# Optimization experiments

Measured on AMD Instinct MI355X. Metric: run time of the kernel, lower is better.

## Reference

```python
import jax, jax.numpy as jnp
import numpy as np

H, DH = 8, 32          # heads, per-head dim
C = H * DH             # channels = 256
N = 20000              # nodes
E = 160000             # edges per relation
L = 4                  # layers
R = 2                  # edge types


def setup_inputs() -> dict:
    key = jax.random.key(0)
    ks = jax.random.split(key, 8)
    return {
        "x": jax.random.normal(ks[0], (N, C), jnp.float32),
        "ei0": jax.random.randint(ks[1], (2, E), 0, N, jnp.int32),
        "ei1": jax.random.randint(ks[2], (2, E), 0, N, jnp.int32),
        "kqv_w": jax.random.normal(ks[3], (L, C, 3 * C), jnp.float32) * 0.05,
        "kqv_b": jnp.zeros((L, 3 * C), jnp.float32),
        "out_w": jax.random.normal(ks[4], (L, C, C), jnp.float32) * 0.05,
        "out_b": jnp.zeros((L, C), jnp.float32),
        "skip": jnp.ones((L,), jnp.float32),
        "krel": jax.random.normal(ks[5], (L, R, H, DH, DH), jnp.float32) * 0.1,
        "vrel": jax.random.normal(ks[6], (L, R, H, DH, DH), jnp.float32) * 0.1,
        "prel": jnp.ones((L, R, H), jnp.float32),
        "ln_g": jnp.ones((L - 1, C), jnp.float32),
        "ln_b": jnp.zeros((L - 1, C), jnp.float32),
    }


def _segment_softmax(logits, seg, n):
    m = jax.ops.segment_max(logits, seg, num_segments=n)
    m = jnp.where(jnp.isfinite(m), m, 0.0)  # empty segments -> avoid -inf
    e = jnp.exp(logits - m[seg])
    s = jax.ops.segment_sum(e, seg, num_segments=n)
    return e / jnp.maximum(s[seg], 1e-16)


def _hgt_conv(x, edge_list, kqv_w, kqv_b, out_w, out_b, skip, krel, vrel, prel):
    n = x.shape[0]
    kqv = x @ kqv_w + kqv_b                       # [N, 3C]
    k, q, v = jnp.split(kqv, 3, axis=1)
    k = k.reshape(n, H, DH)
    q = q.reshape(n, H, DH)
    v = v.reshape(n, H, DH)
    logits, msgs, dsts = [], [], []
    for r, ei in enumerate(edge_list):            # loop over fixed small relation set
        src, dst = ei[0], ei[1]
        k_e = jnp.einsum('ehd,hdf->ehf', k[src], krel[r])   # relation-specific keys
        v_e = jnp.einsum('ehd,hdf->ehf', v[src], vrel[r])   # relation-specific values
        a = (q[dst] * k_e).sum(-1) * prel[r] / np.sqrt(DH)  # [E, H]
        logits.append(a)
        msgs.append(v_e)
        dsts.append(dst)
    logits = jnp.concatenate(logits, 0)
    msgs = jnp.concatenate(msgs, 0)
    dst = jnp.concatenate(dsts, 0)
    # softmax per destination node over ALL incoming edge types jointly (PyG HGTConv)
    alpha = _segment_softmax(logits, dst, n)      # [Etot, H]
    agg = jax.ops.segment_sum(msgs * alpha[:, :, None], dst, num_segments=n)
    agg = agg.reshape(n, C)
    a_out = jax.nn.gelu(agg, approximate=False) @ out_w + out_b
    s = jax.nn.sigmoid(skip)                      # skip applies: out dim == in dim
    return s * a_out + (1.0 - s) * x


def _layer_norm(h, g, b, eps=1e-5):
    mu = h.mean(-1, keepdims=True)
    var = ((h - mu) ** 2).mean(-1, keepdims=True)
    return (h - mu) * jax.lax.rsqrt(var + eps) * g + b


def reference(x, ei0, ei1, kqv_w, kqv_b, out_w, out_b, skip, krel, vrel, prel, ln_g, ln_b):
    edge_list = [ei0, ei1]
    h = x
    for i in range(L):
        h = _hgt_conv(h, edge_list, kqv_w[i], kqv_b[i], out_w[i], out_b[i],
                      skip[i], krel[i], vrel[i], prel[i])
        if i < L - 1:
            h = jax.nn.relu(h)
            h = _layer_norm(h, ln_g[i], ln_b[i])
            # dropout: identity in eval mode (p irrelevant at inference)
    return h
```

## Files before the change

kernel.cpp:

```cpp
#include <hip/hip_runtime.h>
#include <math.h>

#define NN 20000
#define NPAD 20096
#define CC 256
#define HH 8
#define EE 160000
#define TE 320000
#define KVSTRIDE 512
#define APAN ((size_t)NPAD*32)
#define BPAN 40960
#define OPAN 8192

typedef unsigned short u16;
typedef unsigned char u8;
typedef __attribute__((ext_vector_type(8))) short bf16x8;
typedef __attribute__((ext_vector_type(4))) float f32x4;
typedef __attribute__((ext_vector_type(2))) float f32x2;

__device__ __forceinline__ float gelu_exact(float x){
    return 0.5f*x*(1.0f+erff(x*0.7071067811865476f));
}
__device__ __forceinline__ u16 f2bf(float f){
    unsigned u = __float_as_uint(f);
    unsigned r = (u + 0x7fffu + ((u >> 16) & 1u)) >> 16;
    return (u16)r;
}
__device__ __forceinline__ uint2 enc8_fp8(const float* f){
    int t0 = __builtin_amdgcn_cvt_pk_fp8_f32(f[0], f[1], 0, false);
    t0     = __builtin_amdgcn_cvt_pk_fp8_f32(f[2], f[3], t0, true);
    int t1 = __builtin_amdgcn_cvt_pk_fp8_f32(f[4], f[5], 0, false);
    t1     = __builtin_amdgcn_cvt_pk_fp8_f32(f[6], f[7], t1, true);
    uint2 r; r.x = (unsigned)t0; r.y = (unsigned)t1;
    return r;
}
__device__ __forceinline__ void gload_lds16(const u16* gsrc, u16* lds_dst){
    __builtin_amdgcn_global_load_lds((const __attribute__((address_space(1))) unsigned int*)gsrc,
                                     (__attribute__((address_space(3))) unsigned int*)lds_dst,
                                     16, 0, 0);
}

__global__ void hist_k(const int* __restrict__ ei0, const int* __restrict__ ei1,
                       int* __restrict__ cnt){
    int e = blockIdx.x*256 + threadIdx.x;
    if (e < TE){
        int dst = (e < EE) ? ei0[EE + e] : ei1[EE + (e - EE)];
        atomicAdd(&cnt[dst], 1);
    }
}
__global__ void scan_block_k(const int* __restrict__ cnt, int* __restrict__ incl,
                             int* __restrict__ bsum){
    __shared__ int tmp[256];
    int tid = threadIdx.x;
    int i = blockIdx.x*256 + tid;
    int v = (i < NN) ? cnt[i] : 0;
    tmp[tid] = v;
    __syncthreads();
    for (int d=1; d<256; d<<=1){
        int t = (tid>=d) ? tmp[tid-d] : 0;
        __syncthreads();
        tmp[tid] += t;
        __syncthreads();
    }
    if (i < NN) incl[i] = tmp[tid];
    if (tid == 255) bsum[blockIdx.x] = tmp[255];
}
__global__ void finalize_rowptr_k(const int* __restrict__ cnt, const int* __restrict__ incl,
                                  const int* __restrict__ bsum, int* __restrict__ row_ptr){
    __shared__ int wsum[4];
    int tid = threadIdx.x;
    int bid = blockIdx.x;
    int v = (tid < bid) ? bsum[tid] : 0;
    #pragma unroll
    for (int d=1; d<64; d<<=1) v += __shfl_xor(v, d);
    if ((tid & 63) == 0) wsum[tid >> 6] = v;
    __syncthreads();
    int bpre = wsum[0] + wsum[1] + wsum[2] + wsum[3];
    int i = bid*256 + tid;
    if (i < NN) row_ptr[i] = incl[i] - cnt[i] + bpre;
    if (i == NN) row_ptr[NN] = TE;
}
__global__ void scatter_k(const int* __restrict__ ei0, const int* __restrict__ ei1,
                          const int* __restrict__ row_ptr, int* __restrict__ cursor,
                          int* __restrict__ epk){
    int e = blockIdx.x*256 + threadIdx.x;
    if (e < TE){
        int src, dst, rel;
        if (e < EE){ src = ei0[e]; dst = ei0[EE+e]; rel = 0; }
        else { int ee=e-EE; src = ei1[ee]; dst = ei1[EE+ee]; rel = 1; }
        int pos = atomicAdd(&cursor[dst], 1);
        epk[row_ptr[dst] + pos] = rel*NN + src;
    }
}

__global__ void prep_k(const float* __restrict__ kqv_w, const float* __restrict__ kqv_b,
                       const float* __restrict__ krel, const float* __restrict__ vrel,
                       const float* __restrict__ prel, const float* __restrict__ out_w,
                       const float* __restrict__ x,
                       u16* __restrict__ Wt, u16* __restrict__ xbf, u16* __restrict__ Wto,
                       float* __restrict__ bias5, float* __restrict__ sc5,
                       int* __restrict__ cnt, int* __restrict__ cursor){
    int b = blockIdx.x;
    int tid = threadIdx.x;
    if (b < 1024){
        int l = b >> 8, n = b & 255;
        int k = tid;
        const float* W = kqv_w + (size_t)l*196608;
        float val = W[k*768 + 256 + n];
        Wt[(size_t)l*327680 + (size_t)(k>>5)*BPAN + n*32 + (k&31)] = f2bf(val);
    } else if (b < 1152){
        int b2 = b - 1024;
        int l = b2 >> 5;
        int g = (b2 >> 3) & 3;
        int h = b2 & 7;
        int r = g & 1, isv = g >> 1;
        __shared__ float Rs[32*36];
        const float* Rm = (isv ? vrel : krel) + ((size_t)l*2 + r)*8192 + h*1024;
        #pragma unroll
        for (int j=0; j<4; ++j){
            int idx = tid + 256*j;
            Rs[(idx>>5)*36 + (idx&31)] = Rm[idx];
        }
        __syncthreads();
        int base = isv ? 512 : 0;
        const float* W = kqv_w + (size_t)l*196608 + (size_t)tid*768 + base + h*32;
        float w[32];
        #pragma unroll 8
        for (int d=0; d<32; ++d) w[d] = W[d];
        f32x4 acc4[8];
        #pragma unroll
        for (int fb=0; fb<8; ++fb) acc4[fb] = (f32x4){0.f,0.f,0.f,0.f};
        for (int d=0; d<32; ++d){
            float wd = w[d];
            f32x4 wv = (f32x4){wd,wd,wd,wd};
            #pragma unroll
            for (int fb=0; fb<8; ++fb){
                f32x4 rv = *(const f32x4*)&Rs[d*36 + fb*4];
                acc4[fb] += wv * rv;
            }
        }
        int nb = 256 + g*256 + h*32;
        size_t wbase = (size_t)l*327680 + (size_t)(tid>>5)*BPAN + (size_t)(tid&31);
        #pragma unroll
        for (int fb=0; fb<8; ++fb)
            #pragma unroll
            for (int e=0; e<4; ++e)
                Wt[wbase + (size_t)(nb + fb*4 + e)*32] = f2bf(acc4[fb][e]);
    } else if (b < 3652){
        int idx = (b-1152)*256 + tid;
        int e = idx*8;
        int row = e >> 8, col = e & 255;
        const float4* xp = (const float4*)x;
        float4 a = xp[(size_t)idx*2], bb = xp[(size_t)idx*2+1];
        uint4 o;
        o.x = (unsigned)f2bf(a.x) | ((unsigned)f2bf(a.y)<<16);
        o.y = (unsigned)f2bf(a.z) | ((unsigned)f2bf(a.w)<<16);
        o.z = (unsigned)f2bf(bb.x) | ((unsigned)f2bf(bb.y)<<16);
        o.w = (unsigned)f2bf(bb.z) | ((unsigned)f2bf(bb.w)<<16);
        *(uint4*)&xbf[(size_t)(col>>5)*APAN + (size_t)row*32 + (col&31)] = o;
    } else if (b < 4676){
        int idx = (b-3652)*256 + tid;
        int k = idx & 255;
        int n = (idx >> 8) & 255;
        int l = idx >> 16;
        Wto[(size_t)l*65536 + (size_t)(k>>5)*OPAN + n*32 + (k&31)] =
            f2bf(out_w[(size_t)l*65536 + k*256 + n]);
    } else if (b < 4696){
        int idx = (b-4676)*256 + tid;
        int n = idx % 1280, l = idx / 1280;
        const float* B = kqv_b + l*768;
        float val, scl = 1.f;
        if (n < 256) val = B[256+n];
        else {
            int g = (n-256) >> 8;
            int r = g & 1, isv = g >> 1;
            int c = (n-256) & 255;
            int h = c >> 5, f = c & 31;
            const float* Rm = (isv ? vrel : krel) + ((size_t)l*2 + r)*8192 + h*1024;
            int base = isv ? 512 : 0;
            float a = 0.f;
            for (int d=0; d<32; ++d) a += B[base + h*32 + d] * Rm[d*32 + f];
            val = a;
            if (!isv) scl = prel[l*16 + r*8 + h] * 0.17677669529663687f;
        }
        bias5[idx] = val;
        sc5[idx] = scl;
    } else {
        int idx = (b-4696)*256 + tid;
        int4 z; z.x = 0; z.y = 0; z.z = 0; z.w = 0;
        if (idx < 5000)       ((int4*)cnt)[idx] = z;
        else if (idx < 10000) ((int4*)cursor)[idx-5000] = z;
    }
}

__global__ __launch_bounds__(256) void gemm5_k(const u16* __restrict__ A,
        const u16* __restrict__ Wt, const float* __restrict__ biasp,
        const float* __restrict__ sc5p,
        u16* __restrict__ qb, u8* __restrict__ kvb){
    int L = blockIdx.x;
    int xcd = L & 7;
    int t = L >> 3;
    int ytile = xcd*20 + t/10;
    int xtile = t % 10;
    if (ytile >= 157) return;
    int col0 = xtile * 128;
    int row0 = ytile * 128;

    __shared__ __align__(16) char smem[33792];
    u16* As = (u16*)smem;
    u16* Bs = (u16*)(smem + 16384);
    float* Cs = (float*)smem;
    int tid = threadIdx.x;
    int w = tid >> 6, lane = tid & 63;
    int wm = w & 1, wn = w >> 1;
    f32x4 acc[4][4];
    #pragma unroll
    for (int i=0;i<4;++i)
        #pragma unroll
        for (int j=0;j<4;++j) acc[i][j] = (f32x4){0.f,0.f,0.f,0.f};

    int lm = lane & 15, quad = lane >> 4;
    int kq0 = quad ^ (lm & 3);
    int aoff = (wm*64 + lm)*32 + kq0*8;
    int boff = (wn*64 + lm)*32 + kq0*8;

    for (int kk = 0; kk < 4; ++kk){
        #pragma unroll
        for (int hf = 0; hf < 2; ++hf){
            int pan = kk*2 + hf;
            #pragma unroll
            for (int it = 0; it < 2; ++it){
                int s = w*128 + it*64 + lane;
                int row = s >> 2, q0 = s & 3;
                int kq = q0 ^ (row & 3);
                gload_lds16(&A [(size_t)pan*APAN + (size_t)(row0+row)*32 + kq*8],
                            &As[(size_t)(hf*4096) + (size_t)(w*128 + it*64)*8]);
                gload_lds16(&Wt[(size_t)pan*BPAN + (size_t)(col0+row)*32 + kq*8],
                            &Bs[(size_t)(hf*4096) + (size_t)(w*128 + it*64)*8]);
            }
        }
        __syncthreads();
        #pragma unroll
        for (int hf = 0; hf < 2; ++hf){
            bf16x8 af[4], bfr[4];
            #pragma unroll
            for (int mi=0; mi<4; ++mi) af[mi]  = *(bf16x8*)&As[hf*4096 + aoff + mi*512];
            #pragma unroll
            for (int ni=0; ni<4; ++ni) bfr[ni] = *(bf16x8*)&Bs[hf*4096 + boff + ni*512];
            #pragma unroll
            for (int mi=0; mi<4; ++mi)
                #pragma unroll
                for (int ni=0; ni<4; ++ni)
                    acc[mi][ni] = __builtin_amdgcn_mfma_f32_16x16x32_bf16(af[mi], bfr[ni], acc[mi][ni], 0,0,0);
        }
        __syncthreads();
    }

    int bufi = col0 >> 8;
    int cbase = col0 & 255;
    float bvv[4], scv[4];
    #pragma unroll
    for (int ni=0; ni<4; ++ni){
        bvv[ni] = biasp[col0 + wn*64 + ni*16 + lm];
        scv[ni] = sc5p [col0 + wn*64 + ni*16 + lm];
    }

    int rowl_s = tid >> 3;
    int col8   = tid & 7;
    int gcb    = (col8 >> 2)*64 + (col8 & 3)*8;

    #pragma unroll
    for (int p=0; p<2; ++p){
        if (p) __syncthreads();
        #pragma unroll
        for (int nj=0; nj<2; ++nj){
            int ni = p*2 + nj;
            int lcol = wn*32 + nj*16 + lm;
            #pragma unroll
            for (int mi=0; mi<4; ++mi){
                #pragma unroll
                for (int t2=0; t2<4; ++t2){
                    int lr = wm*64 + mi*16 + quad*4 + t2;
                    Cs[lr*66 + lcol] = (acc[mi][ni][t2] + bvv[ni]) * scv[ni];
                }
            }
        }
        __syncthreads();
        int cw = cbase + gcb + p*32;
        #pragma unroll
        for (int it=0; it<4; ++it){
            int rl = rowl_s + it*32;
            int r = row0 + rl;
            if (r < NN){
                const float* src = &Cs[rl*66 + col8*8];
                float cf[8];
                *(float4*)&cf[0] = *(const float4*)&src[0];
                *(float4*)&cf[4] = *(const float4*)&src[4];
                if (bufi == 0){
                    uint4 o;
                    o.x = (unsigned)f2bf(cf[0]) | ((unsigned)f2bf(cf[1])<<16);
                    o.y = (unsigned)f2bf(cf[2]) | ((unsigned)f2bf(cf[3])<<16);
                    o.z = (unsigned)f2bf(cf[4]) | ((unsigned)f2bf(cf[5])<<16);
                    o.w = (unsigned)f2bf(cf[6]) | ((unsigned)f2bf(cf[7])<<16);
                    *(uint4*)&qb[(size_t)r*256 + cw] = o;
                } else if (bufi <= 2){
                    int rel = bufi - 1;
                    uint2 o = enc8_fp8(cf);
                    *(uint2*)&kvb[(size_t)(rel*NN + r)*KVSTRIDE + cw*2] = o;
                } else {
                    int rel = bufi - 3;
                    uint2 o = enc8_fp8(cf);
                    *(uint2*)&kvb[(size_t)(rel*NN + r)*KVSTRIDE + cw*2 + 8] = o;
                }
            }
        }
    }
}

__global__ __launch_bounds__(256) void attn_k(const u16* __restrict__ qb,
        const u8* __restrict__ kvb,
        const int* __restrict__ row_ptr, const int* __restrict__ epk,
        u16* __restrict__ A2){
    int wv = threadIdx.x >> 6, lane = threadIdx.x & 63;
    int node = blockIdx.x*4 + wv;
    int l32 = lane & 31;
    int half = lane >> 5;
    int start = row_ptr[node], end = row_ptr[node+1];
    f32x2 qf[4];
    {
        uint4 qr = *(const uint4*)&qb[(size_t)node*256 + l32*8];
        qf[0] = (f32x2){__uint_as_float(qr.x<<16), __uint_as_float(qr.x&0xffff0000u)};
        qf[1] = (f32x2){__uint_as_float(qr.y<<16), __uint_as_float(qr.y&0xffff0000u)};
        qf[2] = (f32x2){__uint_as_float(qr.z<<16), __uint_as_float(qr.z&0xffff0000u)};
        qf[3] = (f32x2){__uint_as_float(qr.w<<16), __uint_as_float(qr.w&0xffff0000u)};
    }
    float m = -1e30f, s = 0.f;
    f32x2 acc[4];
    #pragma unroll
    for (int j=0;j<4;++j) acc[j] = (f32x2){0.f,0.f};

    int i0 = start + half;
    uint4 c0={0,0,0,0}, c1={0,0,0,0}, c2={0,0,0,0};
    if (i0     < end) c0 = *(const uint4*)&kvb[(size_t)epk[i0  ]*KVSTRIDE + l32*16];
    if (i0 + 2 < end) c1 = *(const uint4*)&kvb[(size_t)epk[i0+2]*KVSTRIDE + l32*16];
    if (i0 + 4 < end) c2 = *(const uint4*)&kvb[(size_t)epk[i0+4]*KVSTRIDE + l32*16];
    int pk = (i0 + 6 < end) ? epk[i0+6] : 0;

    for (int i = i0; i < end; i += 2){
        uint4 cc = c0; c0 = c1; c1 = c2;
        if (i + 6 < end)
            c2 = *(const uint4*)&kvb[(size_t)pk*KVSTRIDE + l32*16];
        if (i + 8 < end) pk = epk[i+8];
        f32x2 kf0 = __builtin_amdgcn_cvt_pk_f32_fp8(cc.x, false);
        f32x2 kf1 = __builtin_amdgcn_cvt_pk_f32_fp8(cc.x, true);
        f32x2 kf2 = __builtin_amdgcn_cvt_pk_f32_fp8(cc.y, false);
        f32x2 kf3 = __builtin_amdgcn_cvt_pk_f32_fp8(cc.y, true);
        f32x2 p2 = qf[0]*kf0 + qf[1]*kf1 + qf[2]*kf2 + qf[3]*kf3;
        float p = p2.x + p2.y;
        p += __shfl_xor(p, 1);
        p += __shfl_xor(p, 2);
        float mo = m;
        m = fmaxf(m, p);
        float sc = __expf(mo - m);
        float pe = __expf(p - m);
        s = s*sc + pe;
        f32x2 vf0 = __builtin_amdgcn_cvt_pk_f32_fp8(cc.z, false);
        f32x2 vf1 = __builtin_amdgcn_cvt_pk_f32_fp8(cc.z, true);
        f32x2 vf2 = __builtin_amdgcn_cvt_pk_f32_fp8(cc.w, false);
        f32x2 vf3 = __builtin_amdgcn_cvt_pk_f32_fp8(cc.w, true);
        f32x2 sc2 = (f32x2){sc,sc}, pe2 = (f32x2){pe,pe};
        acc[0] = acc[0]*sc2 + pe2*vf0;
        acc[1] = acc[1]*sc2 + pe2*vf1;
        acc[2] = acc[2]*sc2 + pe2*vf2;
        acc[3] = acc[3]*sc2 + pe2*vf3;
    }
    float mO = __shfl_xor(m, 32);
    float mA = fmaxf(m, mO);
    float eS = __expf(m - mA);
    float sh = s * eS;
    float sA = sh + __shfl_xor(sh, 32);
    float rs = 1.f / fmaxf(sA, 1e-16f);
    float oA[8];
    #pragma unroll
    for (int j=0;j<4;++j){
        f32x2 a = acc[j] * (f32x2){eS,eS};
        oA[2*j]   = a.x + __shfl_xor(a.x, 32);
        oA[2*j+1] = a.y + __shfl_xor(a.y, 32);
    }
    if (half == 0){
        u16 o[8];
        #pragma unroll
        for (int j=0;j<8;++j) o[j] = f2bf(gelu_exact(oA[j]*rs));
        uint4 ov;
        ov.x = (unsigned)o[0] | ((unsigned)o[1]<<16);
        ov.y = (unsigned)o[2] | ((unsigned)o[3]<<16);
        ov.z = (unsigned)o[4] | ((unsigned)o[5]<<16);
        ov.w = (unsigned)o[6] | ((unsigned)o[7]<<16);
        int c0b = l32*8;
        *(uint4*)&A2[(size_t)(c0b>>5)*APAN + (size_t)node*32 + (c0b&31)] = ov;
    }
}

__global__ __launch_bounds__(256) void gemmOln_k(const u16* __restrict__ A,
        const u16* __restrict__ Wt, const float* __restrict__ bias,
        const float* __restrict__ h_in, const float* __restrict__ skip_l,
        const float* __restrict__ g, const float* __restrict__ b,
        float* __restrict__ h_out, u16* __restrict__ hbf){
    __shared__ __align__(16) char smem[36864];
    u16* As = (u16*)smem;
    u16* Bs = (u16*)(smem + 4096);
    float* part_s = (float*)smem;
    float* part_q = part_s + 32*66;
    float* mu_s   = part_q + 32*66;
    float* rstd_s = mu_s + 32;
    int tid = threadIdx.x;
    int w = tid >> 6, lane = tid & 63;
    int row0 = blockIdx.x * 32;
    f32x4 acc[2][4];
    #pragma unroll
    for (int i=0;i<2;++i)
        #pragma unroll
        for (int j=0;j<4;++j) acc[i][j] = (f32x4){0.f,0.f,0.f,0.f};

    int lm = lane & 15, quad = lane >> 4;
    int kq0 = quad ^ (lm & 3);
    int aoff = lm*32 + kq0*8;
    int boff = (w*64 + lm)*32 + kq0*8;

    for (int kk2 = 0; kk2 < 4; ++kk2){
        {
            int s = tid;
            int hf = s >> 7;
            int s7 = s & 127;
            int row = s7 >> 2, q0 = s7 & 3;
            int kq = q0 ^ (row & 3);
            gload_lds16(&A[(size_t)(kk2*2+hf)*APAN + (size_t)(row0+row)*32 + kq*8],
                        &As[(size_t)(w*64)*8]);
        }
        #pragma unroll
        for (int it = 0; it < 8; ++it){
            int s = it*256 + tid;
            int hf = s >> 10;
            int s10 = s & 1023;
            int row = s10 >> 2, q0 = s10 & 3;
            int kq = q0 ^ (row & 3);
            gload_lds16(&Wt[(size_t)(kk2*2+hf)*OPAN + (size_t)row*32 + kq*8],
                        &Bs[(size_t)(it*256 + w*64)*8]);
        }
        __syncthreads();
        #pragma unroll
        for (int hf = 0; hf < 2; ++hf){
            bf16x8 af[2], bfr[4];
            #pragma unroll
            for (int mi=0; mi<2; ++mi) af[mi]  = *(bf16x8*)&As[hf*1024 + aoff + mi*512];
            #pragma unroll
            for (int ni=0; ni<4; ++ni) bfr[ni] = *(bf16x8*)&Bs[hf*8192 + boff + ni*512];
            #pragma unroll
            for (int mi=0; mi<2; ++mi)
                #pragma unroll
                for (int ni=0; ni<4; ++ni)
                    acc[mi][ni] = __builtin_amdgcn_mfma_f32_16x16x32_bf16(af[mi], bfr[ni], acc[mi][ni], 0,0,0);
        }
        __syncthreads();
    }

    float sskip = 1.f/(1.f+__expf(-skip_l[0]));
    float osk = 1.f - sskip;
    float bv[4], gv[4], bbv[4];
    #pragma unroll
    for (int ni=0; ni<4; ++ni){
        int colg = w*64 + ni*16 + lm;
        bv[ni]  = bias[colg];
        gv[ni]  = g[colg];
        bbv[ni] = b[colg];
    }
    #pragma unroll
    for (int mi=0; mi<2; ++mi){
        #pragma unroll
        for (int t=0; t<4; ++t){
            int lr = mi*16 + quad*4 + t;
            int r = row0 + lr;
            float ps = 0.f, pq = 0.f;
            #pragma unroll
            for (int ni=0; ni<4; ++ni){
                int colg = w*64 + ni*16 + lm;
                float hv = h_in[(size_t)r*256 + colg];
                float val = sskip*(acc[mi][ni][t] + bv[ni]) + osk*hv;
                val = fmaxf(val, 0.f);
                acc[mi][ni][t] = val;
                ps += val; pq += val*val;
            }
            part_s[lr*66 + w*16 + lm] = ps;
            part_q[lr*66 + w*16 + lm] = pq;
        }
    }
    __syncthreads();
    if (tid < 32){
        float S = 0.f, Q = 0.f;
        #pragma unroll 8
        for (int t2=0; t2<64; ++t2){
            S += part_s[tid*66 + t2];
            Q += part_q[tid*66 + t2];
        }
        float mu = S * (1.f/256.f);
        float var = Q * (1.f/256.f) - mu*mu;
        mu_s[tid] = mu;
        rstd_s[tid] = rsqrtf(var + 1e-5f);
    }
    __syncthreads();
    #pragma unroll
    for (int mi=0; mi<2; ++mi){
        #pragma unroll
        for (int t=0; t<4; ++t){
            int lr = mi*16 + quad*4 + t;
            int r = row0 + lr;
            float mu = mu_s[lr], rstd = rstd_s[lr];
            #pragma unroll
            for (int ni=0; ni<4; ++ni){
                int colg = w*64 + ni*16 + lm;
                float o = (acc[mi][ni][t] - mu)*rstd*gv[ni] + bbv[ni];
                h_out[(size_t)r*256 + colg] = o;
                hbf[(size_t)(colg>>5)*APAN + (size_t)r*32 + (colg&31)] = f2bf(o);
            }
        }
    }
}

__global__ __launch_bounds__(256) void gemmO_k(const u16* __restrict__ A,
        const u16* __restrict__ Wt, const float* __restrict__ bias,
        const float* __restrict__ h_in, const float* __restrict__ skip_l,
        float* __restrict__ outp){
    __shared__ u16 As[2048];
    __shared__ u16 Bs[4096];
    int tid = threadIdx.x;
    int w = tid >> 6, lane = tid & 63;
    int row0 = blockIdx.x * 64;
    int col0 = blockIdx.y * 128;
    int wm = w & 1, wn = w >> 1;
    f32x4 acc[2][4];
    #pragma unroll
    for (int i=0;i<2;++i)
        #pragma unroll
        for (int j=0;j<4;++j) acc[i][j] = (f32x4){0.f,0.f,0.f,0.f};

    int lm = lane & 15, quad = lane >> 4;
    int kq0 = quad ^ (lm & 3);
    int aoff = (wm*32 + lm)*32 + kq0*8;
    int boff = (wn*64 + lm)*32 + kq0*8;

    for (int kk = 0; kk < 8; ++kk){
        {
            int s = tid;
            int row = s >> 2, q0 = s & 3;
            int kq = q0 ^ (row & 3);
            gload_lds16(&A[(size_t)kk*APAN + (size_t)(row0+row)*32 + kq*8],
                        &As[(size_t)(w*64)*8]);
        }
        #pragma unroll
        for (int it = 0; it < 2; ++it){
            int s = it*256 + tid;
            int row = s >> 2, q0 = s & 3;
            int kq = q0 ^ (row & 3);
            gload_lds16(&Wt[(size_t)kk*OPAN + (size_t)(col0+row)*32 + kq*8],
                        &Bs[(size_t)(it*256 + w*64)*8]);
        }
        __syncthreads();
        bf16x8 af[2], bfr[4];
        #pragma unroll
        for (int mi=0; mi<2; ++mi) af[mi]  = *(bf16x8*)&As[aoff + mi*512];
        #pragma unroll
        for (int ni=0; ni<4; ++ni) bfr[ni] = *(bf16x8*)&Bs[boff + ni*512];
        #pragma unroll
        for (int mi=0; mi<2; ++mi)
            #pragma unroll
            for (int ni=0; ni<4; ++ni)
                acc[mi][ni] = __builtin_amdgcn_mfma_f32_16x16x32_bf16(af[mi], bfr[ni], acc[mi][ni], 0,0,0);
        __syncthreads();
    }
    float s = 1.f/(1.f+expf(-skip_l[0]));
    float os = 1.f - s;
    #pragma unroll
    for (int ni=0; ni<4; ++ni){
        int colg = col0 + wn*64 + ni*16 + lm;
        float bv = bias[colg];
        #pragma unroll
        for (int mi=0; mi<2; ++mi){
            #pragma unroll
            for (int t=0; t<4; ++t){
                int r = row0 + wm*32 + mi*16 + quad*4 + t;
                if (r < NN)
                    outp[(size_t)r*256 + colg] =
                        s*(acc[mi][ni][t] + bv) + os*h_in[(size_t)r*256 + colg];
            }
        }
    }
}

extern "C" void kernel_launch(void* const* d_in, const int* in_sizes, int n_in,
                              void* d_out, int out_size, void* d_ws, size_t ws_size,
                              hipStream_t stream){
    (void)in_sizes; (void)n_in; (void)out_size; (void)ws_size;
    const float* x     = (const float*)d_in[0];
    const int*   ei0   = (const int*)d_in[1];
    const int*   ei1   = (const int*)d_in[2];
    const float* kqv_w = (const float*)d_in[3];
    const float* kqv_b = (const float*)d_in[4];
    const float* out_w = (const float*)d_in[5];
    const float* out_b = (const float*)d_in[6];
    const float* skip  = (const float*)d_in[7];
    const float* krel  = (const float*)d_in[8];
    const float* vrel  = (const float*)d_in[9];
    const float* prel  = (const float*)d_in[10];
    const float* ln_g  = (const float*)d_in[11];
    const float* ln_b  = (const float*)d_in[12];
    float* outp = (float*)d_out;

    char* wp = (char*)d_ws;
    auto alloc = [&](size_t bytes)->void*{
        void* p = wp; wp += (bytes + 255) & ~(size_t)255; return p;
    };
    float* hA    = (float*)alloc((size_t)NN*CC*4);
    float* hB    = (float*)alloc((size_t)NN*CC*4);
    u16*   xbf   = (u16*)alloc((size_t)NPAD*CC*2);
    u16*   hbf   = (u16*)alloc((size_t)NPAD*CC*2);
    u16*   A2    = (u16*)alloc((size_t)NPAD*CC*2);
    u16*   qb    = (u16*)alloc((size_t)NN*CC*2);
    u8*    kvb   = (u8*)alloc((size_t)2*NN*KVSTRIDE);
    u16*   Wt5   = (u16*)alloc((size_t)4*1280*256*2);
    u16*   Wto   = (u16*)alloc((size_t)4*256*256*2);
    float* bias5 = (float*)alloc((size_t)4*1280*4);
    float* sc5   = (float*)alloc((size_t)4*1280*4);
    int* cnt     = (int*)alloc((size_t)NN*4);
    int* cursor  = (int*)alloc((size_t)NN*4);
    int* incl    = (int*)alloc((size_t)NN*4);
    int* row_ptr = (int*)alloc((size_t)(NN+1)*4);
    int* bsum    = (int*)alloc(128*4);
    int* epk     = (int*)alloc((size_t)TE*4);

    prep_k<<<4736,256,0,stream>>>(kqv_w, kqv_b, krel, vrel, prel, out_w, x,
                                  Wt5, xbf, Wto, bias5, sc5, cnt, cursor);

    hist_k<<<1250,256,0,stream>>>(ei0, ei1, cnt);
    scan_block_k<<<79,256,0,stream>>>(cnt, incl, bsum);
    finalize_rowptr_k<<<79,256,0,stream>>>(cnt, incl, bsum, row_ptr);
    scatter_k<<<1250,256,0,stream>>>(ei0, ei1, row_ptr, cursor, epk);

    const float* h_in = x;
    const u16*   Ain  = xbf;
    float* houts[4] = {hA, hB, hA, outp};
    for (int l=0; l<4; ++l){
        gemm5_k<<<1600,256,0,stream>>>(Ain, Wt5 + (size_t)l*327680,
                bias5 + l*1280, sc5 + l*1280, qb, kvb);
        attn_k<<<5000,256,0,stream>>>(qb, kvb, row_ptr, epk, A2);
        if (l < 3){
            gemmOln_k<<<625,256,0,stream>>>(A2, Wto + (size_t)l*65536,
                    out_b + l*256, h_in, skip + l, ln_g + l*256, ln_b + l*256,
                    houts[l], hbf);
        } else {
            gemmO_k<<<dim3(313,2),256,0,stream>>>(A2, Wto + (size_t)l*65536,
                    out_b + l*256, h_in, skip + l, outp);
        }
        h_in = houts[l];
        Ain = hbf;
    }
}
```

Before: 357.5 us.

## Fuse CSR build into one cooperative kernel and unroll attention edge loop by two

Replaces the four CSR construction kernels (histogram, block scan, row-pointer finalize, scatter) and the counter zeroing in prep with a single cooperative kernel that uses grid-wide syncs between phases, removing several launch gaps. Separately, the attention kernel's per-edge loop now processes two edges per iteration with a deeper four-entry prefetch, merging the online-softmax rescale across both edges. This trades launch overhead for grid sync cost on a small 256-block grid and raises register pressure in the attention kernel.

Result: slower. 470.1 us (+31.5%).

```diff
diff --git a/kernel.cpp b/kernel.cpp
--- a/kernel.cpp
+++ b/kernel.cpp
@@ -1,5 +1,8 @@
 #include <hip/hip_runtime.h>
+#include <hip/hip_cooperative_groups.h>
 #include <math.h>
+
+namespace cg = cooperative_groups;
 
 #define NN 20000
 #define NPAD 20096
@@ -40,56 +43,66 @@
                                      16, 0, 0);
 }
 
-__global__ void hist_k(const int* __restrict__ ei0, const int* __restrict__ ei1,
-                       int* __restrict__ cnt){
-    int e = blockIdx.x*256 + threadIdx.x;
-    if (e < TE){
-        int dst = (e < EE) ? ei0[EE + e] : ei1[EE + (e - EE)];
-        atomicAdd(&cnt[dst], 1);
-    }
-}
-__global__ void scan_block_k(const int* __restrict__ cnt, int* __restrict__ incl,
-                             int* __restrict__ bsum){
+__global__ void csr_coop_k(const int* __restrict__ ei0, const int* __restrict__ ei1,
+                           int* __restrict__ cnt, int* __restrict__ cursor,
+                           int* __restrict__ bsum, int* __restrict__ row_ptr,
+                           int* __restrict__ epk){
+    cg::grid_group grid = cg::this_grid();
+    int tid = threadIdx.x, bid = blockIdx.x;
+    int gt = bid*256 + tid;
+    int4 z; z.x=0; z.y=0; z.z=0; z.w=0;
+    if (gt < 5000)            ((int4*)cnt)[gt] = z;
+    else if (gt < 10000)      ((int4*)cursor)[gt-5000] = z;
+    grid.sync();
+    #pragma unroll
+    for (int it=0; it<5; ++it){
+        int e = gt + it*65536;
+        if (e < TE){
+            int dst = (e < EE) ? ei0[EE + e] : ei1[EE + (e - EE)];
+            atomicAdd(&cnt[dst], 1);
+        }
+    }
+    grid.sync();
     __shared__ int tmp[256];
-    int tid = threadIdx.x;
-    int i = blockIdx.x*256 + tid;
-    int v = (i < NN) ? cnt[i] : 0;
-    tmp[tid] = v;
-    __syncthreads();
-    for (int d=1; d<256; d<<=1){
-        int t = (tid>=d) ? tmp[tid-d] : 0;
-        __syncthreads();
-        tmp[tid] += t;
-        __syncthreads();
-    }
-    if (i < NN) incl[i] = tmp[tid];
-    if (tid == 255) bsum[blockIdx.x] = tmp[255];
-}
-__global__ void finalize_rowptr_k(const int* __restrict__ cnt, const int* __restrict__ incl,
-                                  const int* __restrict__ bsum, int* __restrict__ row_ptr){
     __shared__ int wsum[4];
-    int tid = threadIdx.x;
-    int bid = blockIdx.x;
-    int v = (tid < bid) ? bsum[tid] : 0;
-    #pragma unroll
-    for (int d=1; d<64; d<<=1) v += __shfl_xor(v, d);
-    if ((tid & 63) == 0) wsum[tid >> 6] = v;
-    __syncthreads();
-    int bpre = wsum[0] + wsum[1] + wsum[2] + wsum[3];
-    int i = bid*256 + tid;
-    if (i < NN) row_ptr[i] = incl[i] - cnt[i] + bpre;
-    if (i == NN) row_ptr[NN] = TE;
-}
-__global__ void scatter_k(const int* __restrict__ ei0, const int* __restrict__ ei1,
-                          const int* __restrict__ row_ptr, int* __restrict__ cursor,
-                          int* __restrict__ epk){
-    int e = blockIdx.x*256 + threadIdx.x;
-    if (e < TE){
-        int src, dst, rel;
-        if (e < EE){ src = ei0[e]; dst = ei0[EE+e]; rel = 0; }
-        else { int ee=e-EE; src = ei1[ee]; dst = ei1[EE+ee]; rel = 1; }
-        int pos = atomicAdd(&cursor[dst], 1);
-        epk[row_ptr[dst] + pos] = rel*NN + src;
+    int myc = 0, incl_l = 0;
+    if (bid < 79){
+        int i = bid*256 + tid;
+        myc = (i < NN) ? cnt[i] : 0;
+        tmp[tid] = myc;
+        __syncthreads();
+        for (int d=1; d<256; d<<=1){
+            int t = (tid>=d) ? tmp[tid-d] : 0;
+            __syncthreads();
+            tmp[tid] += t;
+            __syncthreads();
+        }
+        incl_l = tmp[tid];
+        if (tid == 255) bsum[bid] = incl_l;
+    }
+    grid.sync();
+    if (bid < 79){
+        int v = (tid < bid) ? bsum[tid] : 0;
+        #pragma unroll
+        for (int d=1; d<64; d<<=1) v += __shfl_xor(v, d);
+        if ((tid & 63) == 0) wsum[tid >> 6] = v;
+        __syncthreads();
+        int bpre = wsum[0] + wsum[1] + wsum[2] + wsum[3];
+        int i = bid*256 + tid;
+        if (i < NN) row_ptr[i] = incl_l - myc + bpre;
+        if (i == NN) row_ptr[NN] = TE;
+    }
+    grid.sync();
+    #pragma unroll
+    for (int it=0; it<5; ++it){
+        int e = gt + it*65536;
+        if (e < TE){
+            int src, dst, rel;
+            if (e < EE){ src = ei0[e]; dst = ei0[EE+e]; rel = 0; }
+            else { int ee=e-EE; src = ei1[ee]; dst = ei1[EE+ee]; rel = 1; }
+            int pos = atomicAdd(&cursor[dst], 1);
+            epk[row_ptr[dst] + pos] = rel*NN + src;
+        }
     }
 }
 
@@ -98,8 +111,7 @@
                        const float* __restrict__ prel, const float* __restrict__ out_w,
                        const float* __restrict__ x,
                        u16* __restrict__ Wt, u16* __restrict__ xbf, u16* __restrict__ Wto,
-                       float* __restrict__ bias5, float* __restrict__ sc5,
-                       int* __restrict__ cnt, int* __restrict__ cursor){
+                       float* __restrict__ bias5, float* __restrict__ sc5){
     int b = blockIdx.x;
     int tid = threadIdx.x;
     if (b < 1024){
@@ -165,7 +177,7 @@
         int l = idx >> 16;
         Wto[(size_t)l*65536 + (size_t)(k>>5)*OPAN + n*32 + (k&31)] =
             f2bf(out_w[(size_t)l*65536 + k*256 + n]);
-    } else if (b < 4696){
+    } else {
         int idx = (b-4676)*256 + tid;
         int n = idx % 1280, l = idx / 1280;
         const float* B = kqv_b + l*768;
@@ -185,11 +197,6 @@
         }
         bias5[idx] = val;
         sc5[idx] = scl;
-    } else {
-        int idx = (b-4696)*256 + tid;
-        int4 z; z.x = 0; z.y = 0; z.z = 0; z.w = 0;
-        if (idx < 5000)       ((int4*)cnt)[idx] = z;
-        else if (idx < 10000) ((int4*)cursor)[idx-5000] = z;
     }
 }
 
@@ -340,39 +347,70 @@
     for (int j=0;j<4;++j) acc[j] = (f32x2){0.f,0.f};
 
     int i0 = start + half;
-    uint4 c0={0,0,0,0}, c1={0,0,0,0}, c2={0,0,0,0};
+    uint4 c0={0,0,0,0}, c1={0,0,0,0}, c2={0,0,0,0}, c3={0,0,0,0};
     if (i0     < end) c0 = *(const uint4*)&kvb[(size_t)epk[i0  ]*KVSTRIDE + l32*16];
     if (i0 + 2 < end) c1 = *(const uint4*)&kvb[(size_t)epk[i0+2]*KVSTRIDE + l32*16];
     if (i0 + 4 < end) c2 = *(const uint4*)&kvb[(size_t)epk[i0+4]*KVSTRIDE + l32*16];
-    int pk = (i0 + 6 < end) ? epk[i0+6] : 0;
-
-    for (int i = i0; i < end; i += 2){
-        uint4 cc = c0; c0 = c1; c1 = c2;
-        if (i + 6 < end)
-            c2 = *(const uint4*)&kvb[(size_t)pk*KVSTRIDE + l32*16];
-        if (i + 8 < end) pk = epk[i+8];
-        f32x2 kf0 = __builtin_amdgcn_cvt_pk_f32_fp8(cc.x, false);
-        f32x2 kf1 = __builtin_amdgcn_cvt_pk_f32_fp8(cc.x, true);
-        f32x2 kf2 = __builtin_amdgcn_cvt_pk_f32_fp8(cc.y, false);
-        f32x2 kf3 = __builtin_amdgcn_cvt_pk_f32_fp8(cc.y, true);
-        f32x2 p2 = qf[0]*kf0 + qf[1]*kf1 + qf[2]*kf2 + qf[3]*kf3;
-        float p = p2.x + p2.y;
+    if (i0 + 6 < end) c3 = *(const uint4*)&kvb[(size_t)epk[i0+6]*KVSTRIDE + l32*16];
+    int pk8  = (i0 + 8  < end) ? epk[i0+8]  : 0;
+    int pk10 = (i0 + 10 < end) ? epk[i0+10] : 0;
+
+    int i = i0;
+    while (i + 2 < end){
+        uint4 ca = c0, cb = c1;
+        c0 = c2; c1 = c3;
+        if (i + 8  < end) c2 = *(const uint4*)&kvb[(size_t)pk8 *KVSTRIDE + l32*16];
+        if (i + 10 < end) c3 = *(const uint4*)&kvb[(size_t)pk10*KVSTRIDE + l32*16];
+        if (i + 12 < end) pk8  = epk[i+12];
+        if (i + 14 < end) pk10 = epk[i+14];
+        f32x2 pa = qf[0]*__builtin_amdgcn_cvt_pk_f32_fp8(ca.x,false)
+                 + qf[1]*__builtin_amdgcn_cvt_pk_f32_fp8(ca.x,true)
+                 + qf[2]*__builtin_amdgcn_cvt_pk_f32_fp8(ca.y,false)
+                 + qf[3]*__builtin_amdgcn_cvt_pk_f32_fp8(ca.y,true);
+        f32x2 pb = qf[0]*__builtin_amdgcn_cvt_pk_f32_fp8(cb.x,false)
+                 + qf[1]*__builtin_amdgcn_cvt_pk_f32_fp8(cb.x,true)
+                 + qf[2]*__builtin_amdgcn_cvt_pk_f32_fp8(cb.y,false)
+                 + qf[3]*__builtin_amdgcn_cvt_pk_f32_fp8(cb.y,true);
+        float p1 = pa.x + pa.y;
+        float p2 = pb.x + pb.y;
+        p1 += __shfl_xor(p1, 1);  p2 += __shfl_xor(p2, 1);
+        p1 += __shfl_xor(p1, 2);  p2 += __shfl_xor(p2, 2);
+        float mn = fmaxf(m, fmaxf(p1, p2));
+        float sc  = __expf(m - mn);
+        float pe1 = __expf(p1 - mn);
+        float pe2 = __expf(p2 - mn);
+        s = s*sc + pe1 + pe2;
+        m = mn;
+        f32x2 sc2 = (f32x2){sc,sc}, q1 = (f32x2){pe1,pe1}, q2 = (f32x2){pe2,pe2};
+        acc[0] = acc[0]*sc2 + q1*__builtin_amdgcn_cvt_pk_f32_fp8(ca.z,false)
+                            + q2*__builtin_amdgcn_cvt_pk_f32_fp8(cb.z,false);
+        acc[1] = acc[1]*sc2 + q1*__builtin_amdgcn_cvt_pk_f32_fp8(ca.z,true)
+                            + q2*__builtin_amdgcn_cvt_pk_f32_fp8(cb.z,true);
+        acc[2] = acc[2]*sc2 + q1*__builtin_amdgcn_cvt_pk_f32_fp8(ca.w,false)
+                            + q2*__builtin_amdgcn_cvt_pk_f32_fp8(cb.w,false);
+        acc[3] = acc[3]*sc2 + q1*__builtin_amdgcn_cvt_pk_f32_fp8(ca.w,true)
+                            + q2*__builtin_amdgcn_cvt_pk_f32_fp8(cb.w,true);
+        i += 4;
+    }
+    if (i < end){
+        uint4 ca = c0;
+        f32x2 pa = qf[0]*__builtin_amdgcn_cvt_pk_f32_fp8(ca.x,false)
+                 + qf[1]*__builtin_amdgcn_cvt_pk_f32_fp8(ca.x,true)
+                 + qf[2]*__builtin_amdgcn_cvt_pk_f32_fp8(ca.y,false)
+                 + qf[3]*__builtin_amdgcn_cvt_pk_f32_fp8(ca.y,true);
+        float p = pa.x + pa.y;
         p += __shfl_xor(p, 1);
         p += __shfl_xor(p, 2);
-        float mo = m;
-        m = fmaxf(m, p);
-        float sc = __expf(mo - m);
-        float pe = __expf(p - m);
+        float mn = fmaxf(m, p);
+        float sc = __expf(m - mn);
+        float pe = __expf(p - mn);
         s = s*sc + pe;
-        f32x2 vf0 = __builtin_amdgcn_cvt_pk_f32_fp8(cc.z, false);
-        f32x2 vf1 = __builtin_amdgcn_cvt_pk_f32_fp8(cc.z, true);
-        f32x2 vf2 = __builtin_amdgcn_cvt_pk_f32_fp8(cc.w, false);
-        f32x2 vf3 = __builtin_amdgcn_cvt_pk_f32_fp8(cc.w, true);
-        f32x2 sc2 = (f32x2){sc,sc}, pe2 = (f32x2){pe,pe};
-        acc[0] = acc[0]*sc2 + pe2*vf0;
-        acc[1] = acc[1]*sc2 + pe2*vf1;
-        acc[2] = acc[2]*sc2 + pe2*vf2;
-        acc[3] = acc[3]*sc2 + pe2*vf3;
+        m = mn;
+        f32x2 sc2 = (f32x2){sc,sc}, q1 = (f32x2){pe,pe};
+        acc[0] = acc[0]*sc2 + q1*__builtin_amdgcn_cvt_pk_f32_fp8(ca.z,false);
+        acc[1] = acc[1]*sc2 + q1*__builtin_amdgcn_cvt_pk_f32_fp8(ca.z,true);
+        acc[2] = acc[2]*sc2 + q1*__builtin_amdgcn_cvt_pk_f32_fp8(ca.w,false);
+        acc[3] = acc[3]*sc2 + q1*__builtin_amdgcn_cvt_pk_f32_fp8(ca.w,true);
     }
     float mO = __shfl_xor(m, 32);
     float mA = fmaxf(m, mO);
@@ -632,18 +670,19 @@
     float* sc5   = (float*)alloc((size_t)4*1280*4);
     int* cnt     = (int*)alloc((size_t)NN*4);
     int* cursor  = (int*)alloc((size_t)NN*4);
-    int* incl    = (int*)alloc((size_t)NN*4);
     int* row_ptr = (int*)alloc((size_t)(NN+1)*4);
     int* bsum    = (int*)alloc(128*4);
     int* epk     = (int*)alloc((size_t)TE*4);
 
-    prep_k<<<4736,256,0,stream>>>(kqv_w, kqv_b, krel, vrel, prel, out_w, x,
-                                  Wt5, xbf, Wto, bias5, sc5, cnt, cursor);
-
-    hist_k<<<1250,256,0,stream>>>(ei0, ei1, cnt);
-    scan_block_k<<<79,256,0,stream>>>(cnt, incl, bsum);
-    finalize_rowptr_k<<<79,256,0,stream>>>(cnt, incl, bsum, row_ptr);
-    scatter_k<<<1250,256,0,stream>>>(ei0, ei1, row_ptr, cursor, epk);
+    prep_k<<<4696,256,0,stream>>>(kqv_w, kqv_b, krel, vrel, prel, out_w, x,
+                                  Wt5, xbf, Wto, bias5, sc5);
+
+    {
+        void* cargs[7] = {(void*)&ei0, (void*)&ei1, (void*)&cnt, (void*)&cursor,
+                          (void*)&bsum, (void*)&row_ptr, (void*)&epk};
+        hipLaunchCooperativeKernel((const void*)csr_coop_k, dim3(256), dim3(256),
+                                   cargs, 0, stream);
+    }
 
     const float* h_in = x;
     const u16*   Ain  = xbf;
```

## Shrink LDS footprint of QKV and output GEMM kernels to raise occupancy

Applied to the files above, without the earlier changes.

The QKV GEMM epilogue now stages results through LDS in four narrower passes of 16 columns per wave instead of two passes of 32, so the staging buffer fits inside the existing 32 KB A/B tile area. The output-projection GEMM with fused layer norm now stages one K-slice of 32 per iteration over 8 iterations instead of two slices over 4, halving its shared memory. Both changes aim to let more workgroups reside per CU. The cost is extra barriers and more loop iterations with less work between each sync, which may reduce latency hiding.

Result: slower. 369.9 us (+3.5%).

```diff
diff --git a/kernel.cpp b/kernel.cpp
--- a/kernel.cpp
+++ b/kernel.cpp
@@ -206,7 +206,7 @@
     int col0 = xtile * 128;
     int row0 = ytile * 128;
 
-    __shared__ __align__(16) char smem[33792];
+    __shared__ __align__(16) char smem[32768];
     u16* As = (u16*)smem;
     u16* Bs = (u16*)(smem + 16384);
     float* Cs = (float*)smem;
@@ -265,34 +265,29 @@
         scv[ni] = sc5p [col0 + wn*64 + ni*16 + lm];
     }
 
-    int rowl_s = tid >> 3;
-    int col8   = tid & 7;
-    int gcb    = (col8 >> 2)*64 + (col8 & 3)*8;
-
-    #pragma unroll
-    for (int p=0; p<2; ++p){
-        if (p) __syncthreads();
-        #pragma unroll
-        for (int nj=0; nj<2; ++nj){
-            int ni = p*2 + nj;
-            int lcol = wn*32 + nj*16 + lm;
-            #pragma unroll
-            for (int mi=0; mi<4; ++mi){
-                #pragma unroll
-                for (int t2=0; t2<4; ++t2){
-                    int lr = wm*64 + mi*16 + quad*4 + t2;
-                    Cs[lr*66 + lcol] = (acc[mi][ni][t2] + bvv[ni]) * scv[ni];
-                }
+    int rowl_s = tid >> 2;
+    int col4   = tid & 3;
+    int lcolw  = wn*16 + lm;
+
+    #pragma unroll
+    for (int p2=0; p2<4; ++p2){
+        if (p2) __syncthreads();
+        #pragma unroll
+        for (int mi=0; mi<4; ++mi){
+            #pragma unroll
+            for (int t2=0; t2<4; ++t2){
+                int lr = wm*64 + mi*16 + quad*4 + t2;
+                Cs[lr*35 + lcolw] = (acc[mi][p2][t2] + bvv[p2]) * scv[p2];
             }
         }
         __syncthreads();
-        int cw = cbase + gcb + p*32;
-        #pragma unroll
-        for (int it=0; it<4; ++it){
-            int rl = rowl_s + it*32;
+        int cw = cbase + (col4>>1)*64 + (col4&1)*8 + p2*16;
+        #pragma unroll
+        for (int it=0; it<2; ++it){
+            int rl = rowl_s + it*64;
             int r = row0 + rl;
             if (r < NN){
-                const float* src = &Cs[rl*66 + col8*8];
+                const float* src = &Cs[rl*35 + col4*8];
                 float cf[8];
                 *(float4*)&cf[0] = *(const float4*)&src[0];
                 *(float4*)&cf[4] = *(const float4*)&src[4];
@@ -406,9 +401,9 @@
         const float* __restrict__ h_in, const float* __restrict__ skip_l,
         const float* __restrict__ g, const float* __restrict__ b,
         float* __restrict__ h_out, u16* __restrict__ hbf){
-    __shared__ __align__(16) char smem[36864];
+    __shared__ __align__(16) char smem[18432];
     u16* As = (u16*)smem;
-    u16* Bs = (u16*)(smem + 4096);
+    u16* Bs = (u16*)(smem + 2048);
     float* part_s = (float*)smem;
     float* part_q = part_s + 32*66;
     float* mu_s   = part_q + 32*66;
@@ -427,40 +422,32 @@
     int aoff = lm*32 + kq0*8;
     int boff = (w*64 + lm)*32 + kq0*8;
 
-    for (int kk2 = 0; kk2 < 4; ++kk2){
-        {
-            int s = tid;
-            int hf = s >> 7;
-            int s7 = s & 127;
-            int row = s7 >> 2, q0 = s7 & 3;
+    for (int kk = 0; kk < 8; ++kk){
+        if (tid < 128){
+            int row = tid >> 2, q0 = tid & 3;
             int kq = q0 ^ (row & 3);
-            gload_lds16(&A[(size_t)(kk2*2+hf)*APAN + (size_t)(row0+row)*32 + kq*8],
+            gload_lds16(&A[(size_t)kk*APAN + (size_t)(row0+row)*32 + kq*8],
                         &As[(size_t)(w*64)*8]);
         }
         #pragma unroll
-        for (int it = 0; it < 8; ++it){
+        for (int it = 0; it < 4; ++it){
             int s = it*256 + tid;
-            int hf = s >> 10;
-            int s10 = s & 1023;
-            int row = s10 >> 2, q0 = s10 & 3;
+            int row = s >> 2, q0 = s & 3;
             int kq = q0 ^ (row & 3);
-            gload_lds16(&Wt[(size_t)(kk2*2+hf)*OPAN + (size_t)row*32 + kq*8],
+            gload_lds16(&Wt[(size_t)kk*OPAN + (size_t)row*32 + kq*8],
                         &Bs[(size_t)(it*256 + w*64)*8]);
         }
         __syncthreads();
-        #pragma unroll
-        for (int hf = 0; hf < 2; ++hf){
-            bf16x8 af[2], bfr[4];
-            #pragma unroll
-            for (int mi=0; mi<2; ++mi) af[mi]  = *(bf16x8*)&As[hf*1024 + aoff + mi*512];
-            #pragma unroll
-            for (int ni=0; ni<4; ++ni) bfr[ni] = *(bf16x8*)&Bs[hf*8192 + boff + ni*512];
-            #pragma unroll
-            for (int mi=0; mi<2; ++mi)
-                #pragma unroll
-                for (int ni=0; ni<4; ++ni)
-                    acc[mi][ni] = __builtin_amdgcn_mfma_f32_16x16x32_bf16(af[mi], bfr[ni], acc[mi][ni], 0,0,0);
-        }
+        bf16x8 af[2], bfr[4];
+        #pragma unroll
+        for (int mi=0; mi<2; ++mi) af[mi]  = *(bf16x8*)&As[aoff + mi*512];
+        #pragma unroll
+        for (int ni=0; ni<4; ++ni) bfr[ni] = *(bf16x8*)&Bs[boff + ni*512];
+        #pragma unroll
+        for (int mi=0; mi<2; ++mi)
+            #pragma unroll
+            for (int ni=0; ni<4; ++ni)
+                acc[mi][ni] = __builtin_amdgcn_mfma_f32_16x16x32_bf16(af[mi], bfr[ni], acc[mi][ni], 0,0,0);
         __syncthreads();
     }
 
```

## Double-buffer GEMM K-panels with async LDS loads and vmcnt waits

Applied to the files above, without the earlier changes.

Restructures the QKV GEMM main loop from four stages of two panels each, with a full sync after every load, into an eight-panel loop over two ping-pong LDS buffers. The next panel's global-to-LDS load is issued before computing the current one, and s_waitcnt vmcnt(4) waits only on the older loads. The aim is to overlap global memory latency with MFMA work. In exchange there are more barriers, each panel is a smaller unit of work, and correctness relies on hand-written waitcnt counts.

New measurement: 358.7 us. Within noise of the previous version (+0.3%).

```diff
diff --git a/kernel.cpp b/kernel.cpp
--- a/kernel.cpp
+++ b/kernel.cpp
@@ -207,8 +207,6 @@
     int row0 = ytile * 128;
 
     __shared__ __align__(16) char smem[33792];
-    u16* As = (u16*)smem;
-    u16* Bs = (u16*)(smem + 16384);
     float* Cs = (float*)smem;
     int tid = threadIdx.x;
     int w = tid >> 6, lane = tid & 63;
@@ -224,36 +222,43 @@
     int aoff = (wm*64 + lm)*32 + kq0*8;
     int boff = (wn*64 + lm)*32 + kq0*8;
 
-    for (int kk = 0; kk < 4; ++kk){
-        #pragma unroll
-        for (int hf = 0; hf < 2; ++hf){
-            int pan = kk*2 + hf;
-            #pragma unroll
-            for (int it = 0; it < 2; ++it){
-                int s = w*128 + it*64 + lane;
-                int row = s >> 2, q0 = s & 3;
-                int kq = q0 ^ (row & 3);
-                gload_lds16(&A [(size_t)pan*APAN + (size_t)(row0+row)*32 + kq*8],
-                            &As[(size_t)(hf*4096) + (size_t)(w*128 + it*64)*8]);
-                gload_lds16(&Wt[(size_t)pan*BPAN + (size_t)(col0+row)*32 + kq*8],
-                            &Bs[(size_t)(hf*4096) + (size_t)(w*128 + it*64)*8]);
-            }
-        }
-        __syncthreads();
-        #pragma unroll
-        for (int hf = 0; hf < 2; ++hf){
-            bf16x8 af[4], bfr[4];
-            #pragma unroll
-            for (int mi=0; mi<4; ++mi) af[mi]  = *(bf16x8*)&As[hf*4096 + aoff + mi*512];
-            #pragma unroll
-            for (int ni=0; ni<4; ++ni) bfr[ni] = *(bf16x8*)&Bs[hf*4096 + boff + ni*512];
-            #pragma unroll
-            for (int mi=0; mi<4; ++mi)
-                #pragma unroll
-                for (int ni=0; ni<4; ++ni)
-                    acc[mi][ni] = __builtin_amdgcn_mfma_f32_16x16x32_bf16(af[mi], bfr[ni], acc[mi][ni], 0,0,0);
-        }
-        __syncthreads();
+    int s0 = w*128 + lane;
+    auto STAGE = [&](int pan, int buf){
+        #pragma unroll
+        for (int it = 0; it < 2; ++it){
+            int s = s0 + it*64;
+            int row = s >> 2, q0 = s & 3;
+            int kq = q0 ^ (row & 3);
+            u16* dA = (u16*)(smem + buf*16384) + (size_t)s*8;
+            u16* dB = (u16*)(smem + buf*16384 + 8192) + (size_t)s*8;
+            gload_lds16(&A [(size_t)pan*APAN + (size_t)(row0+row)*32 + kq*8], dA);
+            gload_lds16(&Wt[(size_t)pan*BPAN + (size_t)(col0+row)*32 + kq*8], dB);
+        }
+    };
+
+    STAGE(0, 0);
+    #pragma unroll
+    for (int pan = 0; pan < 8; ++pan){
+        int buf = pan & 1;
+        if (pan < 7) STAGE(pan+1, buf^1);
+        if (pan < 7) asm volatile("s_waitcnt vmcnt(4)" ::: "memory");
+        else         asm volatile("s_waitcnt vmcnt(0)" ::: "memory");
+        __builtin_amdgcn_s_barrier();
+        __builtin_amdgcn_sched_barrier(0);
+        const u16* AsB = (const u16*)(smem + buf*16384);
+        const u16* BsB = (const u16*)(smem + buf*16384 + 8192);
+        bf16x8 af[4], bfr[4];
+        #pragma unroll
+        for (int mi=0; mi<4; ++mi) af[mi]  = *(bf16x8*)&AsB[aoff + mi*512];
+        #pragma unroll
+        for (int ni=0; ni<4; ++ni) bfr[ni] = *(bf16x8*)&BsB[boff + ni*512];
+        #pragma unroll
+        for (int mi=0; mi<4; ++mi)
+            #pragma unroll
+            for (int ni=0; ni<4; ++ni)
+                acc[mi][ni] = __builtin_amdgcn_mfma_f32_16x16x32_bf16(af[mi], bfr[ni], acc[mi][ni], 0,0,0);
+        __builtin_amdgcn_sched_barrier(0);
+        __builtin_amdgcn_s_barrier();
     }
 
     int bufi = col0 >> 8;
```
